# Kernel tuning notes

Measured on AMD Instinct MI355X. Metric: run time of the kernel, lower is better.

## Reference

```python
import jax, jax.numpy as jnp
import numpy as np

N = 100000
E = 3200000
IN_DIM = 512
OUT_DIM = 128


def setup_inputs() -> dict:
    key = jax.random.key(0)
    k1, k2, k3 = jax.random.split(key, 3)
    x = jax.random.normal(k1, (N, IN_DIM), dtype=jnp.float32)
    edge_index = jax.random.randint(k2, (2, E), 0, N, dtype=jnp.int64)
    # Glorot init like PyG GCNConv
    W = jax.random.normal(k3, (IN_DIM, OUT_DIM), dtype=jnp.float32) * (2.0 / (IN_DIM + OUT_DIM)) ** 0.5
    b = jnp.zeros((OUT_DIM,), dtype=jnp.float32)
    return {"x": x, "edge_index": edge_index, "W": W, "b": b}


def gcn_conv(x, edge_index, W, b):
    # GCNConv with add_self_loops=True, normalize=True (symmetric norm)
    row, col = edge_index[0], edge_index[1]  # messages flow row -> col
    xw = x @ W  # [N, out_dim]
    ones = jnp.ones((E,), dtype=xw.dtype)
    # degree of destination nodes, +1 for self-loop
    deg = jax.ops.segment_sum(ones, col, num_segments=N) + 1.0
    dinv = jax.lax.rsqrt(deg)  # deg^{-1/2}, deg >= 1 so no inf
    norm = dinv[row] * dinv[col]  # [E]
    msg = xw[row] * norm[:, None]  # gather + scale
    out = jax.ops.segment_sum(msg, col, num_segments=N)  # scatter-add
    # self-loop contribution: norm_ii = dinv_i * dinv_i
    out = out + xw * (dinv * dinv)[:, None]
    return out + b


def reference(x, edge_index, W, b):
    return gcn_conv(x, edge_index, W, b)
```

## Files before the change

### kernel.cpp

```cpp
#include <hip/hip_runtime.h>

using short8 = __attribute__((ext_vector_type(8))) short;
using f32x4  = __attribute__((ext_vector_type(4))) float;

static constexpr int N_NODES = 100000;
static constexpr int N_EDGES = 3200000;
static constexpr int IN_DIM  = 512;
static constexpr int OUT_DIM = 128;
static constexpr int NBINS   = (N_NODES + 255) / 256;
static constexpr int NB      = 1024;
static constexpr int CHUNK   = N_EDGES / NB;

__device__ __forceinline__ short f2bf(float f) {
  unsigned u = __builtin_bit_cast(unsigned, f);
  u = (u + 0x7FFFu + ((u >> 16) & 1u)) >> 16;
  return (short)u;
}

__global__ __launch_bounds__(256) void cast_WT(const float* __restrict__ W,
                                               short* __restrict__ WT) {
  const int idx = blockIdx.x * 256 + threadIdx.x;
  const int c = idx >> 9, k = idx & 511;
  WT[(size_t)c * 512 + k] = f2bf(W[(size_t)k * 128 + c]);
}

__global__ __launch_bounds__(256) void gemm_mfma(const float* __restrict__ x,
                                                 const short* __restrict__ WT,
                                                 unsigned short* __restrict__ xwb) {
  __shared__ short As[2][64 * 128];
  const int tid  = threadIdx.x;
  const int row0 = blockIdx.x * 64;

  float4 pf[8];

  auto issue_loads = [&](int kb) {
#pragma unroll
    for (int c = 0; c < 4; ++c) {
      const int flat = c * 2048 + tid * 8;
      const int r = flat >> 7;
      const int k = flat & 127;
      const int row = row0 + r;
      if (row < N_NODES) {
        const float* s = &x[(size_t)row * IN_DIM + kb + k];
        pf[c * 2]     = *reinterpret_cast<const float4*>(s);
        pf[c * 2 + 1] = *reinterpret_cast<const float4*>(s + 4);
      } else {
        pf[c * 2]     = make_float4(0.f, 0.f, 0.f, 0.f);
        pf[c * 2 + 1] = make_float4(0.f, 0.f, 0.f, 0.f);
      }
    }
  };

  auto write_lds = [&](int buf) {
#pragma unroll
    for (int c = 0; c < 4; ++c) {
      const int flat = c * 2048 + tid * 8;
      const int r = flat >> 7;
      const int k = flat & 127;
      const float4 f0 = pf[c * 2], f1 = pf[c * 2 + 1];
      short8 sv;
      sv[0] = f2bf(f0.x); sv[1] = f2bf(f0.y); sv[2] = f2bf(f0.z); sv[3] = f2bf(f0.w);
      sv[4] = f2bf(f1.x); sv[5] = f2bf(f1.y); sv[6] = f2bf(f1.z); sv[7] = f2bf(f1.w);
      const int byte = (k * 2) ^ ((r & 7) << 4);
      *reinterpret_cast<short8*>(reinterpret_cast<char*>(As[buf]) + r * 256 + byte) = sv;
    }
  };

  const int l  = tid & 63;
  const int w  = tid >> 6;
  const int wr = w >> 1, wc = w & 1;
  const int lr = l & 15;
  const int lk = l >> 4;

  const int arow0 = wr * 32 + lr;
  const int arow1 = arow0 + 16;
  const int ab0 = arow0 * 256, rx0 = (arow0 & 7) << 4;
  const int ab1 = arow1 * 256, rx1 = (arow1 & 7) << 4;

  const short* bB0 = WT + (size_t)(wc * 64 +  0 + lr) * 512 + lk * 8;
  const short* bB1 = WT + (size_t)(wc * 64 + 16 + lr) * 512 + lk * 8;
  const short* bB2 = WT + (size_t)(wc * 64 + 32 + lr) * 512 + lk * 8;
  const short* bB3 = WT + (size_t)(wc * 64 + 48 + lr) * 512 + lk * 8;

  f32x4 acc[2][4] = {};

  issue_loads(0);
  write_lds(0);
  __syncthreads();

#pragma unroll
  for (int kbidx = 0; kbidx < 4; ++kbidx) {
    const int cur = kbidx & 1;
    if (kbidx < 3) issue_loads((kbidx + 1) * 128);

    const char* base = reinterpret_cast<const char*>(As[cur]);
#pragma unroll
    for (int ks = 0; ks < 4; ++ks) {
      const int kbyte = ks * 64 + lk * 16;
      const short8 a0 = *reinterpret_cast<const short8*>(base + ab0 + (kbyte ^ rx0));
      const short8 a1 = *reinterpret_cast<const short8*>(base + ab1 + (kbyte ^ rx1));
      const int ko = kbidx * 128 + ks * 32;
      const short8 bb0 = *reinterpret_cast<const short8*>(bB0 + ko);
      const short8 bb1 = *reinterpret_cast<const short8*>(bB1 + ko);
      const short8 bb2 = *reinterpret_cast<const short8*>(bB2 + ko);
      const short8 bb3 = *reinterpret_cast<const short8*>(bB3 + ko);
      acc[0][0] = __builtin_amdgcn_mfma_f32_16x16x32_bf16(a0, bb0, acc[0][0], 0, 0, 0);
      acc[0][1] = __builtin_amdgcn_mfma_f32_16x16x32_bf16(a0, bb1, acc[0][1], 0, 0, 0);
      acc[0][2] = __builtin_amdgcn_mfma_f32_16x16x32_bf16(a0, bb2, acc[0][2], 0, 0, 0);
      acc[0][3] = __builtin_amdgcn_mfma_f32_16x16x32_bf16(a0, bb3, acc[0][3], 0, 0, 0);
      acc[1][0] = __builtin_amdgcn_mfma_f32_16x16x32_bf16(a1, bb0, acc[1][0], 0, 0, 0);
      acc[1][1] = __builtin_amdgcn_mfma_f32_16x16x32_bf16(a1, bb1, acc[1][1], 0, 0, 0);
      acc[1][2] = __builtin_amdgcn_mfma_f32_16x16x32_bf16(a1, bb2, acc[1][2], 0, 0, 0);
      acc[1][3] = __builtin_amdgcn_mfma_f32_16x16x32_bf16(a1, bb3, acc[1][3], 0, 0, 0);
    }

    if (kbidx < 3) {
      write_lds(cur ^ 1);
      __syncthreads();
    }
  }

#pragma unroll
  for (int m = 0; m < 2; ++m) {
    const int rbase = row0 + wr * 32 + m * 16 + (l >> 4) * 4;
#pragma unroll
    for (int j = 0; j < 4; ++j) {
      const int row = rbase + j;
      if (row < N_NODES) {
        unsigned short* o = &xwb[(size_t)row * OUT_DIM + wc * 64 + lr];
        o[0]  = (unsigned short)f2bf(acc[m][0][j]);
        o[16] = (unsigned short)f2bf(acc[m][1][j]);
        o[32] = (unsigned short)f2bf(acc[m][2][j]);
        o[48] = (unsigned short)f2bf(acc[m][3][j]);
      }
    }
  }
}


__global__ __launch_bounds__(256) void bin_count(const int* __restrict__ ecol,
                                                 int* __restrict__ blkhist) {
  __shared__ int hist[NBINS];
  const int blk = blockIdx.x, tid = threadIdx.x;
  for (int i = tid; i < NBINS; i += 256) hist[i] = 0;
  __syncthreads();
  const int e0 = blk * CHUNK, e1 = e0 + CHUNK;
  for (int e = e0 + tid; e < e1; e += 256) atomicAdd(&hist[ecol[e] >> 8], 1);
  __syncthreads();
  for (int i = tid; i < NBINS; i += 256) blkhist[(size_t)blk * NBINS + i] = hist[i];
}

__global__ __launch_bounds__(1024) void scan_blkhist(int* __restrict__ blkhist,
                                                     int* __restrict__ bintot) {
  __shared__ int sh[NB];
  const int bin = blockIdx.x, t = threadIdx.x;
  const int v = blkhist[(size_t)t * NBINS + bin];
  sh[t] = v;
  __syncthreads();
  for (int d = 1; d < NB; d <<= 1) {
    const int tv = (t >= d) ? sh[t - d] : 0;
    __syncthreads();
    sh[t] += tv;
    __syncthreads();
  }
  blkhist[(size_t)t * NBINS + bin] = sh[t] - v;
  if (t == NB - 1) bintot[bin] = sh[t];
}

__global__ __launch_bounds__(512) void scan_bins(const int* __restrict__ bintot,
                                                 int* __restrict__ binbase) {
  __shared__ int sh[512];
  const int t = threadIdx.x;
  const int v = (t < NBINS) ? bintot[t] : 0;
  sh[t] = v;
  __syncthreads();
  for (int d = 1; d < 512; d <<= 1) {
    const int tv = (t >= d) ? sh[t - d] : 0;
    __syncthreads();
    sh[t] += tv;
    __syncthreads();
  }
  if (t < NBINS) binbase[t] = sh[t] - v;
  if (t == NBINS - 1) binbase[NBINS] = sh[t];
}

__global__ __launch_bounds__(256) void bin_scatter(const int* __restrict__ erow,
                                                   const int* __restrict__ ecol,
                                                   const int* __restrict__ blkhist,
                                                   const int* __restrict__ binbase,
                                                   int2* __restrict__ benc) {
  __shared__ int cur[NBINS];
  const int blk = blockIdx.x, tid = threadIdx.x;
  for (int i = tid; i < NBINS; i += 256)
    cur[i] = binbase[i] + blkhist[(size_t)blk * NBINS + i];
  __syncthreads();
  const int e0 = blk * CHUNK, e1 = e0 + CHUNK;
  for (int e = e0 + tid; e < e1; e += 256) {
    const int c = ecol[e];
    const int r = erow[e];
    const int p = atomicAdd(&cur[c >> 8], 1);
    benc[p] = make_int2(r, c);
  }
}

__global__ __launch_bounds__(256) void bin_build(const int2* __restrict__ benc,
                                                 const int* __restrict__ binbase,
                                                 int* __restrict__ brow,
                                                 int* __restrict__ offs,
                                                 float* __restrict__ dinv) {
  __shared__ int hist[256];
  __shared__ int sh[256];
  __shared__ int cur[256];
  const int b = blockIdx.x, tid = threadIdx.x;
  const int n0 = b << 8;
  const int e0 = binbase[b], e1 = binbase[b + 1];
  hist[tid] = 0;
  __syncthreads();
  for (int e = e0 + tid; e < e1; e += 256) atomicAdd(&hist[benc[e].y - n0], 1);
  __syncthreads();
  const int d0 = hist[tid];
  sh[tid] = d0;
  __syncthreads();
  for (int d = 1; d < 256; d <<= 1) {
    const int tv = (tid >= d) ? sh[tid - d] : 0;
    __syncthreads();
    sh[tid] += tv;
    __syncthreads();
  }
  const int myoff = e0 + sh[tid] - d0;
  cur[tid] = myoff;
  const int node = n0 + tid;
  if (node < N_NODES) {
    offs[node] = myoff;
    dinv[node] = rsqrtf((float)d0 + 1.0f);
  }
  if (b == NBINS - 1 && tid == 255) offs[N_NODES] = e1;
  __syncthreads();
  for (int e = e0 + tid; e < e1; e += 256) {
    const int2 rc = benc[e];
    const int p = atomicAdd(&cur[rc.y - n0], 1);
    brow[p] = rc.x;
  }
}

__global__ __launch_bounds__(256) void gather_out(const unsigned short* __restrict__ xwb,
                                                  const float* __restrict__ dinv,
                                                  const int* __restrict__ offs,
                                                  const int* __restrict__ brow,
                                                  const float* __restrict__ bias,
                                                  float* __restrict__ out) {
  const int lane = threadIdx.x & 63;
  const int node = blockIdx.x * (blockDim.x >> 6) + (threadIdx.x >> 6);
  if (node >= N_NODES) return;
  const float di = dinv[node];
  const int c0 = lane * 2;

  auto ld2 = [&](int r) -> float2 {
    const unsigned v = *reinterpret_cast<const unsigned*>(&xwb[(size_t)r * OUT_DIM + c0]);
    float2 f;
    f.x = __builtin_bit_cast(float, v << 16);
    f.y = __builtin_bit_cast(float, v & 0xFFFF0000u);
    return f;
  };

  float2 acc;
  {
    const float2 v = ld2(node);
    const float s = di * di;
    acc.x = v.x * s;
    acc.y = v.y * s;
  }

  int e = offs[node];
  const int e1 = offs[node + 1];
  for (; e + 4 <= e1; e += 4) {
    const int r0 = brow[e], r1 = brow[e + 1], r2 = brow[e + 2], r3 = brow[e + 3];
    const float n0 = dinv[r0] * di;
    const float n1 = dinv[r1] * di;
    const float n2 = dinv[r2] * di;
    const float n3 = dinv[r3] * di;
    const float2 v0 = ld2(r0), v1 = ld2(r1), v2 = ld2(r2), v3 = ld2(r3);
    acc.x += v0.x * n0 + v1.x * n1 + v2.x * n2 + v3.x * n3;
    acc.y += v0.y * n0 + v1.y * n1 + v2.y * n2 + v3.y * n3;
  }
  for (; e < e1; ++e) {
    const int r = brow[e];
    const float nr = dinv[r] * di;
    const float2 v = ld2(r);
    acc.x += v.x * nr;
    acc.y += v.y * nr;
  }

  const float2 bb = *reinterpret_cast<const float2*>(&bias[c0]);
  float2 o;
  o.x = acc.x + bb.x;
  o.y = acc.y + bb.y;
  *reinterpret_cast<float2*>(&out[(size_t)node * OUT_DIM + c0]) = o;
}

extern "C" void kernel_launch(void* const* d_in, const int* in_sizes, int n_in,
                              void* d_out, int out_size, void* d_ws, size_t ws_size,
                              hipStream_t stream) {
  const float* x    = (const float*)d_in[0];
  const int*   eidx = (const int*)d_in[1];
  const float* W    = (const float*)d_in[2];
  const float* b    = (const float*)d_in[3];
  float* out = (float*)d_out;

  const int* erow = eidx;
  const int* ecol = eidx + N_EDGES;

  char* ws = (char*)d_ws;
  size_t off = 0;
  auto alloc = [&](size_t bytes) -> void* {
    void* p = ws + off;
    off = (off + bytes + 255) & ~(size_t)255;
    return p;
  };
  unsigned short* xwb = (unsigned short*)alloc((size_t)N_NODES * OUT_DIM * sizeof(short));
  short* WT      = (short*)alloc((size_t)OUT_DIM * IN_DIM * sizeof(short));
  float* dinv    = (float*)alloc((size_t)N_NODES * sizeof(float));
  int*   offs    = (int*)alloc((size_t)(N_NODES + 1) * sizeof(int));
  int*   blkhist = (int*)alloc((size_t)NB * NBINS * sizeof(int));
  int*   bintot  = (int*)alloc((size_t)NBINS * sizeof(int));
  int*   binbase = (int*)alloc((size_t)(NBINS + 1) * sizeof(int));
  int*   brow    = (int*)alloc((size_t)N_EDGES * sizeof(int));
  int2*  benc    = (int2*)alloc((size_t)N_EDGES * sizeof(int2));

  cast_WT<<<256, 256, 0, stream>>>(W, WT);

  bin_count<<<NB, 256, 0, stream>>>(ecol, blkhist);
  scan_blkhist<<<NBINS, NB, 0, stream>>>(blkhist, bintot);
  scan_bins<<<1, 512, 0, stream>>>(bintot, binbase);
  bin_scatter<<<NB, 256, 0, stream>>>(erow, ecol, blkhist, binbase, benc);
  bin_build<<<NBINS, 256, 0, stream>>>(benc, binbase, brow, offs, dinv);

  gemm_mfma<<<(N_NODES + 63) / 64, 256, 0, stream>>>(x, WT, xwb);
  gather_out<<<(N_NODES + 3) / 4, 256, 0, stream>>>(xwb, dinv, offs, brow, b, out);
}
```

Measured before the change: 321.3 us.

## Prescale GEMM rows by dinv and pack bin entries into 32-bit words

```diff
diff --git a/kernel.cpp b/kernel.cpp
--- a/kernel.cpp
+++ b/kernel.cpp
@@ -26,6 +26,7 @@
 
 __global__ __launch_bounds__(256) void gemm_mfma(const float* __restrict__ x,
                                                  const short* __restrict__ WT,
+                                                 const float* __restrict__ dinv,
                                                  unsigned short* __restrict__ xwb) {
   __shared__ short As[2][64 * 128];
   const int tid  = threadIdx.x;
@@ -127,11 +128,12 @@
     for (int j = 0; j < 4; ++j) {
       const int row = rbase + j;
       if (row < N_NODES) {
+        const float sc = dinv[row];
         unsigned short* o = &xwb[(size_t)row * OUT_DIM + wc * 64 + lr];
-        o[0]  = (unsigned short)f2bf(acc[m][0][j]);
-        o[16] = (unsigned short)f2bf(acc[m][1][j]);
-        o[32] = (unsigned short)f2bf(acc[m][2][j]);
-        o[48] = (unsigned short)f2bf(acc[m][3][j]);
+        o[0]  = (unsigned short)f2bf(acc[m][0][j] * sc);
+        o[16] = (unsigned short)f2bf(acc[m][1][j] * sc);
+        o[32] = (unsigned short)f2bf(acc[m][2][j] * sc);
+        o[48] = (unsigned short)f2bf(acc[m][3][j] * sc);
       }
     }
   }
@@ -188,7 +190,7 @@
                                                    const int* __restrict__ ecol,
                                                    const int* __restrict__ blkhist,
                                                    const int* __restrict__ binbase,
-                                                   int2* __restrict__ benc) {
+                                                   unsigned* __restrict__ benc) {
   __shared__ int cur[NBINS];
   const int blk = blockIdx.x, tid = threadIdx.x;
   for (int i = tid; i < NBINS; i += 256)
@@ -197,13 +199,13 @@
   const int e0 = blk * CHUNK, e1 = e0 + CHUNK;
   for (int e = e0 + tid; e < e1; e += 256) {
     const int c = ecol[e];
-    const int r = erow[e];
+    const unsigned enc = (unsigned)erow[e] | ((unsigned)(c & 255) << 24);
     const int p = atomicAdd(&cur[c >> 8], 1);
-    benc[p] = make_int2(r, c);
-  }
-}
-
-__global__ __launch_bounds__(256) void bin_build(const int2* __restrict__ benc,
+    benc[p] = enc;
+  }
+}
+
+__global__ __launch_bounds__(256) void bin_build(const unsigned* __restrict__ benc,
                                                  const int* __restrict__ binbase,
                                                  int* __restrict__ brow,
                                                  int* __restrict__ offs,
@@ -212,11 +214,10 @@
   __shared__ int sh[256];
   __shared__ int cur[256];
   const int b = blockIdx.x, tid = threadIdx.x;
-  const int n0 = b << 8;
   const int e0 = binbase[b], e1 = binbase[b + 1];
   hist[tid] = 0;
   __syncthreads();
-  for (int e = e0 + tid; e < e1; e += 256) atomicAdd(&hist[benc[e].y - n0], 1);
+  for (int e = e0 + tid; e < e1; e += 256) atomicAdd(&hist[benc[e] >> 24], 1);
   __syncthreads();
   const int d0 = hist[tid];
   sh[tid] = d0;
@@ -229,7 +230,7 @@
   }
   const int myoff = e0 + sh[tid] - d0;
   cur[tid] = myoff;
-  const int node = n0 + tid;
+  const int node = (b << 8) + tid;
   if (node < N_NODES) {
     offs[node] = myoff;
     dinv[node] = rsqrtf((float)d0 + 1.0f);
@@ -237,9 +238,9 @@
   if (b == NBINS - 1 && tid == 255) offs[N_NODES] = e1;
   __syncthreads();
   for (int e = e0 + tid; e < e1; e += 256) {
-    const int2 rc = benc[e];
-    const int p = atomicAdd(&cur[rc.y - n0], 1);
-    brow[p] = rc.x;
+    const unsigned v = benc[e];
+    const int p = atomicAdd(&cur[v >> 24], 1);
+    brow[p] = (int)(v & 0x00FFFFFFu);
   }
 }
 
@@ -263,38 +264,28 @@
     return f;
   };
 
-  float2 acc;
-  {
-    const float2 v = ld2(node);
-    const float s = di * di;
-    acc.x = v.x * s;
-    acc.y = v.y * s;
-  }
+  float2 acc = ld2(node);
 
   int e = offs[node];
   const int e1 = offs[node + 1];
-  for (; e + 4 <= e1; e += 4) {
-    const int r0 = brow[e], r1 = brow[e + 1], r2 = brow[e + 2], r3 = brow[e + 3];
-    const float n0 = dinv[r0] * di;
-    const float n1 = dinv[r1] * di;
-    const float n2 = dinv[r2] * di;
-    const float n3 = dinv[r3] * di;
+  for (; e + 8 <= e1; e += 8) {
+    const int r0 = brow[e],     r1 = brow[e + 1], r2 = brow[e + 2], r3 = brow[e + 3];
+    const int r4 = brow[e + 4], r5 = brow[e + 5], r6 = brow[e + 6], r7 = brow[e + 7];
     const float2 v0 = ld2(r0), v1 = ld2(r1), v2 = ld2(r2), v3 = ld2(r3);
-    acc.x += v0.x * n0 + v1.x * n1 + v2.x * n2 + v3.x * n3;
-    acc.y += v0.y * n0 + v1.y * n1 + v2.y * n2 + v3.y * n3;
+    const float2 v4 = ld2(r4), v5 = ld2(r5), v6 = ld2(r6), v7 = ld2(r7);
+    acc.x += ((v0.x + v1.x) + (v2.x + v3.x)) + ((v4.x + v5.x) + (v6.x + v7.x));
+    acc.y += ((v0.y + v1.y) + (v2.y + v3.y)) + ((v4.y + v5.y) + (v6.y + v7.y));
   }
   for (; e < e1; ++e) {
-    const int r = brow[e];
-    const float nr = dinv[r] * di;
-    const float2 v = ld2(r);
-    acc.x += v.x * nr;
-    acc.y += v.y * nr;
+    const float2 v = ld2(brow[e]);
+    acc.x += v.x;
+    acc.y += v.y;
   }
 
   const float2 bb = *reinterpret_cast<const float2*>(&bias[c0]);
   float2 o;
-  o.x = acc.x + bb.x;
-  o.y = acc.y + bb.y;
+  o.x = acc.x * di + bb.x;
+  o.y = acc.y * di + bb.y;
   *reinterpret_cast<float2*>(&out[(size_t)node * OUT_DIM + c0]) = o;
 }
 
@@ -325,7 +316,7 @@
   int*   bintot  = (int*)alloc((size_t)NBINS * sizeof(int));
   int*   binbase = (int*)alloc((size_t)(NBINS + 1) * sizeof(int));
   int*   brow    = (int*)alloc((size_t)N_EDGES * sizeof(int));
-  int2*  benc    = (int2*)alloc((size_t)N_EDGES * sizeof(int2));
+  unsigned* benc = (unsigned*)alloc((size_t)N_EDGES * sizeof(unsigned));
 
   cast_WT<<<256, 256, 0, stream>>>(W, WT);
 
@@ -335,6 +326,6 @@
   bin_scatter<<<NB, 256, 0, stream>>>(erow, ecol, blkhist, binbase, benc);
   bin_build<<<NBINS, 256, 0, stream>>>(benc, binbase, brow, offs, dinv);
 
-  gemm_mfma<<<(N_NODES + 63) / 64, 256, 0, stream>>>(x, WT, xwb);
+  gemm_mfma<<<(N_NODES + 63) / 64, 256, 0, stream>>>(x, WT, dinv, xwb);
   gather_out<<<(N_NODES + 3) / 4, 256, 0, stream>>>(xwb, dinv, offs, brow, b, out);
 }
```

After: 302.1 us. 6.0% less time.
